# Kernel tuning notes

Hardware: AMD Instinct MI355X
Metric: run time of the kernel (lower is better)

## Reference

```python
import jax, jax.numpy as jnp
import numpy as np

N_MELS = 80
N_MAPS = 128
N_LABELS = 35
INTEGRATION_TIME = 1.0
NSTEPS = 4  # fixed-step RK4 stand-in for adaptive dopri5
BN_EPS = 1e-5


def _conv(x, w, pad_h):
    # x: [B, C, T, 1], w: [O, I, kH, 1]
    return jax.lax.conv_general_dilated(
        x, w, window_strides=(1, 1), padding=[(pad_h, pad_h), (0, 0)],
        dimension_numbers=("NCHW", "OIHW", "NCHW"))


def _bn(x):
    # BatchNorm2d(affine=False) with batch statistics (training-mode math, biased var)
    m = jnp.mean(x, axis=(0, 2, 3), keepdims=True)
    v = jnp.mean(jnp.square(x - m), axis=(0, 2, 3), keepdims=True)
    return (x - m) * jax.lax.rsqrt(v + BN_EPS)


def setup_inputs() -> dict:
    key = jax.random.key(0)
    ks = jax.random.split(key, 7)
    B, T = 128, 500
    def he(k, shape, fan_in):
        return jax.random.normal(k, shape, dtype=jnp.float32) * np.float32(np.sqrt(2.0 / fan_in))
    return {
        "x": jax.random.normal(ks[0], (B, N_MELS, T), dtype=jnp.float32),
        "conv0_w": he(ks[1], (N_MAPS, N_MELS, 3, 1), N_MELS * 3),
        "conv1_w": he(ks[2], (N_MAPS, N_MAPS, 9, 1), N_MAPS * 9),
        "conv2_w": he(ks[3], (N_MAPS, N_MAPS, 9, 1), N_MAPS * 9),
        "conv3_w": he(ks[4], (N_MAPS, N_MAPS, 1, 1), N_MAPS),
        "out_w": he(ks[5], (N_LABELS, N_MAPS), N_MAPS),
        "out_b": jnp.zeros((N_LABELS,), dtype=jnp.float32),
    }


def reference(x, conv0_w, conv1_w, conv2_w, conv3_w, out_w, out_b):
    # x: [B, n_mels, T] -> unsqueeze(3) -> [B, n_mels, T, 1]
    h = x[..., None]
    h = _conv(h, conv0_w, pad_h=1)          # conv0 (3,1), pad (1,0)
    h = jax.nn.relu(_bn(h))                  # norm_in + relu

    def odefunc(z):
        # TCNN_ODEfunc.forward (t only selects BN stats; batch stats used here)
        out = _conv(z, conv1_w, pad_h=4)
        out = jax.nn.relu(_bn(out))
        out = _conv(out, conv2_w, pad_h=4)
        out = _bn(out)
        out3 = jax.nn.relu(_bn(_conv(z, conv3_w, pad_h=0)))
        return jax.nn.relu(out + out3)

    dt = jnp.float32(INTEGRATION_TIME / NSTEPS)

    def rk4_step(z, _):
        k1 = odefunc(z)
        k2 = odefunc(z + 0.5 * dt * k1)
        k3 = odefunc(z + 0.5 * dt * k2)
        k4 = odefunc(z + dt * k3)
        return z + (dt / 6.0) * (k1 + 2.0 * k2 + 2.0 * k3 + k4), None

    h, _ = jax.lax.scan(rk4_step, h, None, length=NSTEPS)

    # global average pool over (T, 1) then linear head
    feat = jnp.mean(h.reshape(h.shape[0], h.shape[1], -1), axis=2)  # [B, n_maps]
    return feat @ out_w.T + out_b
```

## Files before the change

### kernel.cpp

```cpp
#include <hip/hip_runtime.h>
#include <hip/hip_bf16.h>
#include <cstddef>

constexpr int B = 128;
constexpr int T = 500;
constexpr int C = 128;
constexpr int CIN = 80;
constexpr int NL = 35;
constexpr size_t NBCT = (size_t)B * C * T;
constexpr int WPAD = 132;
constexpr int I0 = 96;
constexpr int IPAD0 = 104;
constexpr int NT = 64;
constexpr int NPART = 1024;

typedef __attribute__((ext_vector_type(8))) _Float16 half8;
typedef __attribute__((ext_vector_type(4))) _Float16 half4;
typedef __attribute__((ext_vector_type(4))) float f32x4;

__device__ float g_zA[NBCT];
__device__ float g_zB[NBCT];
__device__ _Float16 g_z16[NBCT];
__device__ _Float16 g_accA[NBCT];
__device__ _Float16 g_accB[NBCT];
__device__ _Float16 g_t1[NBCT];
__device__ _Float16 g_t2[NBCT];
__device__ _Float16 g_t3[NBCT];
__device__ float g_ps1[C * NPART], g_pq1[C * NPART];
__device__ float g_ps2[C * NPART], g_pq2[C * NPART];
__device__ float g_ps3[C * NPART], g_pq3[C * NPART];
__device__ float g_m1[C], g_r1[C], g_m2[C], g_r2[C], g_m3[C], g_r3[C];
__device__ float g_featp[B * 4 * C];
__device__ _Float16 g_w0f[3 * C * I0];
__device__ _Float16 g_w1f[9 * C * C];
__device__ _Float16 g_w2f[9 * C * C];
__device__ _Float16 g_w3f[1 * C * C];

__device__ inline half8 h8zero() {
  half8 v;
#pragma unroll
  for (int j = 0; j < 8; j++) v[j] = (_Float16)0.f;
  return v;
}

__inline__ __device__ float wave_sum(float v) {
  for (int off = 32; off; off >>= 1) v += __shfl_down(v, off);
  return v;
}

__device__ inline void swz_block(int& tile, int& b) {
  int flat = blockIdx.y * 8 + blockIdx.x;
  int swz = (flat & 7) * 128 + (flat >> 3);
  tile = swz & 7;
  b = swz >> 3;
}

template <int KW>
__global__ __launch_bounds__(256) void prep_weights_f16(
    const float* __restrict__ w, _Float16* __restrict__ wf) {
  int idx = blockIdx.x * 256 + threadIdx.x;
  if (idx >= C * C * KW) return;
  int kw = idx % KW;
  int i = (idx / KW) % C;
  int o = idx / (KW * C);
  size_t dst = (((size_t)kw * 16 + (i >> 3)) * C + o) * 8 + (i & 7);
  wf[dst] = (_Float16)w[idx];
}

__global__ __launch_bounds__(256) void prep_w0_f16(
    const float* __restrict__ w, _Float16* __restrict__ wf) {
  int idx = blockIdx.x * 256 + threadIdx.x;
  if (idx >= 3 * C * I0) return;
  int i = idx % I0;
  int o = (idx / I0) % C;
  int kw = idx / (I0 * C);
  float v = 0.f;
  if (i < CIN) v = w[((size_t)o * CIN + i) * 3 + kw];
  wf[((size_t)kw * C + o) * I0 + i] = (_Float16)v;
}

__device__ inline void reduce_one(const float* __restrict__ ps,
                                  const float* __restrict__ pq,
                                  float* __restrict__ om,
                                  float* __restrict__ orr, int c) {
  float s = 0.f, q = 0.f;
  for (int p = threadIdx.x; p < NPART; p += 256) {
    s += ps[c * NPART + p];
    q += pq[c * NPART + p];
  }
  s = wave_sum(s);
  q = wave_sum(q);
  __shared__ float ls[8];
  int wv = threadIdx.x >> 6, ln = threadIdx.x & 63;
  if (ln == 0) { ls[wv] = s; ls[4 + wv] = q; }
  __syncthreads();
  if (threadIdx.x == 0) {
    float S = ls[0] + ls[1] + ls[2] + ls[3];
    float Q = ls[4] + ls[5] + ls[6] + ls[7];
    const float invn = 1.f / 64000.f;
    float m = S * invn;
    float v = Q * invn - m * m;
    om[c] = m;
    orr[c] = rsqrtf(v + 1e-5f);
  }
}

__global__ __launch_bounds__(256) void reduce_stats(
    const float* __restrict__ ps, const float* __restrict__ pq,
    float* __restrict__ om, float* __restrict__ orr) {
  reduce_one(ps, pq, om, orr, blockIdx.x);
}

__global__ __launch_bounds__(256) void reduce_stats2(
    const float* __restrict__ psA, const float* __restrict__ pqA,
    float* __restrict__ omA, float* __restrict__ orA,
    const float* __restrict__ psB, const float* __restrict__ pqB,
    float* __restrict__ omB, float* __restrict__ orB) {
  if (blockIdx.y == 0)
    reduce_one(psA, pqA, omA, orA, blockIdx.x);
  else
    reduce_one(psB, pqB, omB, orB, blockIdx.x);
}

template <int NG, int NTG>
__device__ inline void store_and_stats_f(f32x4 (&dacc)[NG][NTG],
                                         float* __restrict__ outb,
                                         float* __restrict__ ssum,
                                         float* __restrict__ ssq, int tbase,
                                         int og0, int quad, int m15) {
#pragma unroll
  for (int g = 0; g < NG; g++) {
    float rs[4] = {0.f, 0.f, 0.f, 0.f}, rq[4] = {0.f, 0.f, 0.f, 0.f};
#pragma unroll
    for (int tg = 0; tg < NTG; tg++) {
      int t = tbase + tg * 16 + m15;
      bool valid = t < T;
      f32x4 d = dacc[g][tg];
      if (valid)
        *(f32x4*)(outb + (size_t)t * C + (og0 + g) * 16 + quad * 4) = d;
#pragma unroll
      for (int r = 0; r < 4; r++) {
        float v = valid ? d[r] : 0.f;
        rs[r] += v;
        rq[r] += v * v;
      }
    }
#pragma unroll
    for (int sh = 1; sh < 16; sh <<= 1) {
#pragma unroll
      for (int r = 0; r < 4; r++) {
        rs[r] += __shfl_xor(rs[r], sh);
        rq[r] += __shfl_xor(rq[r], sh);
      }
    }
    if (m15 == 0) {
      int o = (og0 + g) * 16 + quad * 4;
#pragma unroll
      for (int r = 0; r < 4; r++) {
        atomicAdd(&ssum[o + r], rs[r]);
        atomicAdd(&ssq[o + r], rq[r]);
      }
    }
  }
}

template <int NG, int NTG>
__device__ inline void store_and_stats_h(f32x4 (&dacc)[NG][NTG],
                                         _Float16* __restrict__ outb,
                                         float* __restrict__ ssum,
                                         float* __restrict__ ssq, int tbase,
                                         int og0, int quad, int m15) {
#pragma unroll
  for (int g = 0; g < NG; g++) {
    float rs[4] = {0.f, 0.f, 0.f, 0.f}, rq[4] = {0.f, 0.f, 0.f, 0.f};
#pragma unroll
    for (int tg = 0; tg < NTG; tg++) {
      int t = tbase + tg * 16 + m15;
      bool valid = t < T;
      f32x4 d = dacc[g][tg];
      if (valid) {
        half4 h;
#pragma unroll
        for (int r = 0; r < 4; r++) h[r] = (_Float16)d[r];
        *(half4*)(outb + (size_t)t * C + (og0 + g) * 16 + quad * 4) = h;
      }
#pragma unroll
      for (int r = 0; r < 4; r++) {
        float v = valid ? d[r] : 0.f;
        rs[r] += v;
        rq[r] += v * v;
      }
    }
#pragma unroll
    for (int sh = 1; sh < 16; sh <<= 1) {
#pragma unroll
      for (int r = 0; r < 4; r++) {
        rs[r] += __shfl_xor(rs[r], sh);
        rq[r] += __shfl_xor(rq[r], sh);
      }
    }
    if (m15 == 0) {
      int o = (og0 + g) * 16 + quad * 4;
#pragma unroll
      for (int r = 0; r < 4; r++) {
        atomicAdd(&ssum[o + r], rs[r]);
        atomicAdd(&ssq[o + r], rq[r]);
      }
    }
  }
}

__global__ __launch_bounds__(256, 4) void conv13f(
    const _Float16* __restrict__ t2g, const _Float16* __restrict__ t3g,
    const float* __restrict__ m2, const float* __restrict__ r2,
    const float* __restrict__ m3, const float* __restrict__ r3,
    const float* __restrict__ zc, _Float16* __restrict__ z16,
    const _Float16* __restrict__ accr, float* __restrict__ zn,
    _Float16* __restrict__ accw, const _Float16* __restrict__ w9,
    const _Float16* __restrict__ w1, _Float16* __restrict__ out1,
    _Float16* __restrict__ out3, float* __restrict__ ps1,
    float* __restrict__ pq1, float* __restrict__ ps3,
    float* __restrict__ pq3, float wacc, float anext, int mode, int initf,
    int finf) {
  constexpr int PAD = 4;
  constexpr int ROWS = NT + 8;
  __shared__ __align__(16) _Float16 sh[ROWS * WPAD];
  __shared__ float ssum1[C], ssq1[C], ssum3[C], ssq3[C];
  __shared__ float sm2[C], sr2[C], sm3[C], sr3[C];

  const int tid = threadIdx.x;
  int tile, b;
  swz_block(tile, b);
  const int t0 = tile * NT;

  if (tid < 128) {
    ssum1[tid] = 0.f; ssq1[tid] = 0.f;
    ssum3[tid] = 0.f; ssq3[tid] = 0.f;
    if (mode) {
      sm2[tid] = m2[tid]; sr2[tid] = r2[tid];
      sm3[tid] = m3[tid]; sr3[tid] = r3[tid];
    }
  }
  __syncthreads();

  for (int e = tid; e < ROWS * 16; e += 256) {
    int r = e >> 4;
    int c8 = e & 15;
    int t = t0 - PAD + r;
    half8 v = h8zero();
    if (t >= 0 && t < T) {
      size_t off = (size_t)b * T * C + (size_t)t * C + c8 * 8;
      if (mode == 0) {
        v = *(const half8*)(z16 + off);
      } else {
        half8 h2 = *(const half8*)(t2g + off);
        half8 h3 = *(const half8*)(t3g + off);
        float zf[8];
        if (finf) {
          float4 z0 = *(const float4*)(zc + off);
          float4 z1 = *(const float4*)(zc + off + 4);
          zf[0] = z0.x; zf[1] = z0.y; zf[2] = z0.z; zf[3] = z0.w;
          zf[4] = z1.x; zf[5] = z1.y; zf[6] = z1.z; zf[7] = z1.w;
        } else {
          half8 hz = *(const half8*)(z16 + off);
#pragma unroll
          for (int j = 0; j < 8; j++) zf[j] = (float)hz[j];
        }
        half8 ha = h8zero();
        if (!initf) ha = *(const half8*)(accr + off);
        int c = c8 * 8;
        float va[8], zo[8];
#pragma unroll
        for (int j = 0; j < 8; j++) {
          float f2 = (float)h2[j];
          float f3 = (float)h3[j];
          float k = fmaxf((f2 - sm2[c + j]) * sr2[c + j] +
                              fmaxf((f3 - sm3[c + j]) * sr3[c + j], 0.f),
                          0.f);
          va[j] = initf ? wacc * k : (float)ha[j] + wacc * k;
          zo[j] = zf[j] + anext * (finf ? va[j] : k);
          v[j] = (_Float16)zo[j];
        }
        bool owned = (r >= PAD) && (r < PAD + NT);
        if (owned) {
          if (finf) {
            *(float4*)(zn + off) = make_float4(zo[0], zo[1], zo[2], zo[3]);
            *(float4*)(zn + off + 4) = make_float4(zo[4], zo[5], zo[6], zo[7]);
            *(half8*)(z16 + off) = v;
          } else {
            half8 aw;
#pragma unroll
            for (int j = 0; j < 8; j++) aw[j] = (_Float16)va[j];
            *(half8*)(accw + off) = aw;
          }
        }
      }
    }
    *(half8*)&sh[r * WPAD + c8 * 8] = v;
  }
  __syncthreads();

  const int wv = tid >> 6;
  const int lane = tid & 63;
  const int quad = lane >> 4;
  const int m15 = lane & 15;
  const int og0 = wv * 2;

  const half8* __restrict__ A9 = (const half8*)w9;
  const half8* __restrict__ A1 = (const half8*)w1;

  {
    f32x4 d3[2][4];
#pragma unroll
    for (int g = 0; g < 2; g++)
#pragma unroll
      for (int tg = 0; tg < 4; tg++) d3[g][tg] = f32x4{0.f, 0.f, 0.f, 0.f};
#pragma unroll
    for (int ic = 0; ic < 4; ic++) {
      const int kof = ic * 32 + quad * 8;
      half8 af[2];
#pragma unroll
      for (int g = 0; g < 2; g++)
        af[g] = A1[(ic * 4 + quad) * C + (og0 + g) * 16 + m15];
      half8 bf[4];
#pragma unroll
      for (int tg = 0; tg < 4; tg++)
        bf[tg] = *(const half8*)(sh + (tg * 16 + m15 + PAD) * WPAD + kof);
#pragma unroll
      for (int g = 0; g < 2; g++)
#pragma unroll
        for (int tg = 0; tg < 4; tg++)
          d3[g][tg] = __builtin_amdgcn_mfma_f32_16x16x32_f16(
              af[g], bf[tg], d3[g][tg], 0, 0, 0);
    }
    _Float16* __restrict__ o3b = out3 + (size_t)b * T * C;
    store_and_stats_h<2, 4>(d3, o3b, ssum3, ssq3, t0, og0, quad, m15);
  }

  f32x4 d1[2][4];
#pragma unroll
  for (int g = 0; g < 2; g++)
#pragma unroll
    for (int tg = 0; tg < 4; tg++) d1[g][tg] = f32x4{0.f, 0.f, 0.f, 0.f};

  for (int kw = 0; kw < 9; kw++) {
#pragma unroll
    for (int ic = 0; ic < 4; ic++) {
      const int kof = ic * 32 + quad * 8;
      half8 af[2];
#pragma unroll
      for (int g = 0; g < 2; g++)
        af[g] = A9[(kw * 16 + ic * 4 + quad) * C + (og0 + g) * 16 + m15];
      half8 bf[4];
#pragma unroll
      for (int tg = 0; tg < 4; tg++)
        bf[tg] = *(const half8*)(sh + (tg * 16 + m15 + kw) * WPAD + kof);
#pragma unroll
      for (int g = 0; g < 2; g++)
#pragma unroll
        for (int tg = 0; tg < 4; tg++)
          d1[g][tg] = __builtin_amdgcn_mfma_f32_16x16x32_f16(
              af[g], bf[tg], d1[g][tg], 0, 0, 0);
    }
  }

  _Float16* __restrict__ o1b = out1 + (size_t)b * T * C;
  store_and_stats_h<2, 4>(d1, o1b, ssum1, ssq1, t0, og0, quad, m15);
  __syncthreads();
  int p = b * 8 + tile;
  if (tid < 128) {
    ps1[tid * NPART + p] = ssum1[tid];
    pq1[tid * NPART + p] = ssq1[tid];
    ps3[tid * NPART + p] = ssum3[tid];
    pq3[tid * NPART + p] = ssq3[tid];
  }
}

__global__ __launch_bounds__(256, 4) void conv2_bn(
    const _Float16* __restrict__ in, const _Float16* __restrict__ wf,
    const float* __restrict__ bnm, const float* __restrict__ bnr,
    _Float16* __restrict__ out, float* __restrict__ ps,
    float* __restrict__ pq) {
  constexpr int KW = 9, PAD = 4;
  constexpr int ROWS = NT + KW - 1;
  __shared__ __align__(16) _Float16 sh[ROWS * WPAD];
  __shared__ float ssum[C], ssq[C];
  __shared__ float sbm[C], sbr[C];

  const int tid = threadIdx.x;
  int tile, b;
  swz_block(tile, b);
  const int t0 = tile * NT;

  if (tid < 128) {
    sbm[tid] = bnm[tid];
    sbr[tid] = bnr[tid];
    ssum[tid] = 0.f;
    ssq[tid] = 0.f;
  }
  __syncthreads();

  const _Float16* __restrict__ inb = in + (size_t)b * T * C;
  for (int e = tid; e < ROWS * 16; e += 256) {
    int r = e >> 4;
    int c8 = e & 15;
    int t = t0 - PAD + r;
    half8 v = h8zero();
    if (t >= 0 && t < T) {
      half8 u = *(const half8*)(inb + (size_t)t * C + c8 * 8);
      int c = c8 * 8;
#pragma unroll
      for (int j = 0; j < 8; j++) {
        float f = (float)u[j];
        f = fmaxf((f - sbm[c + j]) * sbr[c + j], 0.f);
        v[j] = (_Float16)f;
      }
    }
    *(half8*)&sh[r * WPAD + c8 * 8] = v;
  }
  __syncthreads();

  const int wv = tid >> 6;
  const int lane = tid & 63;
  const int quad = lane >> 4;
  const int m15 = lane & 15;
  const int og0 = wv * 2;

  const half8* __restrict__ Af = (const half8*)wf;

  f32x4 dacc[2][4];
#pragma unroll
  for (int g = 0; g < 2; g++)
#pragma unroll
    for (int tg = 0; tg < 4; tg++) dacc[g][tg] = f32x4{0.f, 0.f, 0.f, 0.f};

  for (int kw = 0; kw < 9; kw++) {
#pragma unroll
    for (int ic = 0; ic < 4; ic++) {
      const int kof = ic * 32 + quad * 8;
      half8 af[2];
#pragma unroll
      for (int g = 0; g < 2; g++)
        af[g] = Af[(kw * 16 + ic * 4 + quad) * C + (og0 + g) * 16 + m15];
      half8 bf[4];
#pragma unroll
      for (int tg = 0; tg < 4; tg++)
        bf[tg] = *(const half8*)(sh + (tg * 16 + m15 + kw) * WPAD + kof);
#pragma unroll
      for (int g = 0; g < 2; g++)
#pragma unroll
        for (int tg = 0; tg < 4; tg++)
          dacc[g][tg] = __builtin_amdgcn_mfma_f32_16x16x32_f16(
              af[g], bf[tg], dacc[g][tg], 0, 0, 0);
    }
  }

  _Float16* __restrict__ outb = out + (size_t)b * T * C;
  store_and_stats_h<2, 4>(dacc, outb, ssum, ssq, t0, og0, quad, m15);
  __syncthreads();
  int p = b * 8 + tile;
  if (tid < 128) {
    ps[tid * NPART + p] = ssum[tid];
    pq[tid * NPART + p] = ssq[tid];
  }
}

__global__ __launch_bounds__(256) void conv0_mfma(
    const float* __restrict__ in, const _Float16* __restrict__ wf,
    float* __restrict__ out, float* __restrict__ ps, float* __restrict__ pq) {
  constexpr int KW = 3, PAD = 1;
  constexpr int ROWS = NT + KW - 1;
  __shared__ __align__(16) _Float16 sh[ROWS * IPAD0];
  __shared__ float ssum[C], ssq[C];

  const int tid = threadIdx.x;
  const int tile = blockIdx.x;
  const int b = blockIdx.y;
  const int t0 = tile * NT;

  if (tid < 128) { ssum[tid] = 0.f; ssq[tid] = 0.f; }
  __syncthreads();

  const float* __restrict__ inb = in + (size_t)b * CIN * T;
  for (int e = tid; e < I0 * ROWS; e += 256) {
    int i = e / ROWS;
    int r = e % ROWS;
    int t = t0 - PAD + r;
    float v = 0.f;
    if (i < CIN && t >= 0 && t < T) v = inb[(size_t)i * T + t];
    sh[r * IPAD0 + i] = (_Float16)v;
  }
  __syncthreads();

  const int wv = tid >> 6;
  const int lane = tid & 63;
  const int quad = lane >> 4;
  const int m15 = lane & 15;
  const int og0 = wv * 2;

  f32x4 dacc[2][4];
#pragma unroll
  for (int g = 0; g < 2; g++)
#pragma unroll
    for (int tg = 0; tg < 4; tg++) dacc[g][tg] = f32x4{0.f, 0.f, 0.f, 0.f};

  for (int kw = 0; kw < KW; kw++) {
    const _Float16* __restrict__ wk = wf + (size_t)kw * C * I0;
#pragma unroll
    for (int ic = 0; ic < 3; ic++) {
      const int kof = ic * 32 + quad * 8;
      half8 af[2];
#pragma unroll
      for (int g = 0; g < 2; g++) {
        size_t off = (size_t)((og0 + g) * 16 + m15) * I0 + kof;
        af[g] = *(const half8*)(wk + off);
      }
      half8 bf[4];
#pragma unroll
      for (int tg = 0; tg < 4; tg++) {
        int off = (tg * 16 + m15 + kw) * IPAD0 + kof;
        bf[tg] = *(const half8*)(sh + off);
      }
#pragma unroll
      for (int g = 0; g < 2; g++)
#pragma unroll
        for (int tg = 0; tg < 4; tg++)
          dacc[g][tg] = __builtin_amdgcn_mfma_f32_16x16x32_f16(
              af[g], bf[tg], dacc[g][tg], 0, 0, 0);
    }
  }

  float* __restrict__ outb = out + (size_t)b * T * C;
  store_and_stats_f<2, 4>(dacc, outb, ssum, ssq, t0, og0, quad, m15);
  __syncthreads();
  int p = b * 8 + tile;
  if (tid < 128) {
    ps[tid * NPART + p] = ssum[tid];
    pq[tid * NPART + p] = ssq[tid];
  }
}

__global__ __launch_bounds__(256) void apply_bn_relu(
    float* __restrict__ x, const float* __restrict__ m,
    const float* __restrict__ r, _Float16* __restrict__ zh) {
  __shared__ float sm[C], sr[C];
  if (threadIdx.x < 128) {
    sm[threadIdx.x] = m[threadIdx.x];
    sr[threadIdx.x] = r[threadIdx.x];
  }
  __syncthreads();
  const size_t total4 = NBCT / 4;
  size_t stride = (size_t)gridDim.x * 256;
  for (size_t i4 = (size_t)blockIdx.x * 256 + threadIdx.x; i4 < total4;
       i4 += stride) {
    int c = (int)((i4 & 31) * 4);
    float4 v = ((float4*)x)[i4];
    v.x = fmaxf((v.x - sm[c]) * sr[c], 0.f);
    v.y = fmaxf((v.y - sm[c + 1]) * sr[c + 1], 0.f);
    v.z = fmaxf((v.z - sm[c + 2]) * sr[c + 2], 0.f);
    v.w = fmaxf((v.w - sm[c + 3]) * sr[c + 3], 0.f);
    ((float4*)x)[i4] = v;
    half4 h;
    h[0] = (_Float16)v.x;
    h[1] = (_Float16)v.y;
    h[2] = (_Float16)v.z;
    h[3] = (_Float16)v.w;
    *(half4*)(zh + i4 * 4) = h;
  }
}

__global__ __launch_bounds__(256) void combine_fin(
    const _Float16* __restrict__ t2, const _Float16* __restrict__ t3,
    const float* __restrict__ m2, const float* __restrict__ r2,
    const float* __restrict__ m3, const float* __restrict__ r3,
    float* __restrict__ z, const _Float16* __restrict__ acc, float wacc,
    float anext) {
  __shared__ float sm2[C], sr2[C], sm3[C], sr3[C];
  if (threadIdx.x < 128) {
    sm2[threadIdx.x] = m2[threadIdx.x];
    sr2[threadIdx.x] = r2[threadIdx.x];
    sm3[threadIdx.x] = m3[threadIdx.x];
    sr3[threadIdx.x] = r3[threadIdx.x];
  }
  __syncthreads();
  const size_t total4 = NBCT / 4;
  size_t stride = (size_t)gridDim.x * 256;
  for (size_t i4 = (size_t)blockIdx.x * 256 + threadIdx.x; i4 < total4;
       i4 += stride) {
    int c = (int)((i4 & 31) * 4);
    size_t off = i4 * 4;
    half4 h2 = *(const half4*)(t2 + off);
    half4 h3 = *(const half4*)(t3 + off);
    half4 ha = *(const half4*)(acc + off);
    float4 vz = *(const float4*)(z + off);
    float vzf[4] = {vz.x, vz.y, vz.z, vz.w};
    float vo[4];
#pragma unroll
    for (int j = 0; j < 4; j++) {
      float f2 = (float)h2[j];
      float f3 = (float)h3[j];
      float k = fmaxf((f2 - sm2[c + j]) * sr2[c + j] +
                          fmaxf((f3 - sm3[c + j]) * sr3[c + j], 0.f),
                      0.f);
      float va = (float)ha[j] + wacc * k;
      vo[j] = vzf[j] + anext * va;
    }
    *(float4*)(z + off) = make_float4(vo[0], vo[1], vo[2], vo[3]);
  }
}

__global__ __launch_bounds__(256) void feat_part(
    const float* __restrict__ z, float* __restrict__ fp) {
  const int b = blockIdx.x;
  const int s = blockIdx.y;
  const int c = threadIdx.x & 127;
  const int h = threadIdx.x >> 7;
  const float* zb = z + (size_t)b * T * C;
  float sum = 0.f;
  for (int t = s * 125 + h; t < (s + 1) * 125; t += 2)
    sum += zb[(size_t)t * C + c];
  __shared__ float sf[2][C];
  sf[h][c] = sum;
  __syncthreads();
  if (threadIdx.x < 128)
    fp[((size_t)b * 4 + s) * C + threadIdx.x] =
        sf[0][threadIdx.x] + sf[1][threadIdx.x];
}

__global__ __launch_bounds__(256) void head2(
    const float* __restrict__ fp, const float* __restrict__ ow,
    const float* __restrict__ ob, float* __restrict__ out) {
  const int b = blockIdx.x;
  __shared__ float feat[C];
  if (threadIdx.x < 128) {
    float s = 0.f;
#pragma unroll
    for (int p = 0; p < 4; p++) s += fp[((size_t)b * 4 + p) * C + threadIdx.x];
    feat[threadIdx.x] = s * (1.f / 500.f);
  }
  __syncthreads();
  if (threadIdx.x < NL) {
    int l = threadIdx.x;
    float o = ob[l];
    for (int j = 0; j < C; j++) o = fmaf(feat[j], ow[l * C + j], o);
    out[b * NL + l] = o;
  }
}

extern "C" void kernel_launch(void* const* d_in, const int* in_sizes, int n_in,
                              void* d_out, int out_size, void* d_ws,
                              size_t ws_size, hipStream_t stream) {
  const float* x  = (const float*)d_in[0];
  const float* w0 = (const float*)d_in[1];
  const float* w1 = (const float*)d_in[2];
  const float* w2 = (const float*)d_in[3];
  const float* w3 = (const float*)d_in[4];
  const float* ow = (const float*)d_in[5];
  const float* ob = (const float*)d_in[6];
  float* out = (float*)d_out;

  static float *zA, *zB, *featp;
  static float *ps1, *pq1, *ps2, *pq2, *ps3, *pq3;
  static float *m1, *r1, *m2, *r2, *m3, *r3;
  static _Float16 *z16, *accA, *accB, *t1, *t2, *t3;
  static _Float16 *w0f, *w1f, *w2f, *w3f;
  static bool inited = false;
  if (!inited) {
    void* p;
#define GET(sym, var) hipGetSymbolAddress(&p, HIP_SYMBOL(sym)); var = (decltype(var))p;
    GET(g_zA, zA) GET(g_zB, zB) GET(g_z16, z16)
    GET(g_accA, accA) GET(g_accB, accB)
    GET(g_t1, t1) GET(g_t2, t2) GET(g_t3, t3)
    GET(g_ps1, ps1) GET(g_pq1, pq1) GET(g_ps2, ps2) GET(g_pq2, pq2)
    GET(g_ps3, ps3) GET(g_pq3, pq3)
    GET(g_m1, m1) GET(g_r1, r1) GET(g_m2, m2) GET(g_r2, r2)
    GET(g_m3, m3) GET(g_r3, r3) GET(g_featp, featp)
    GET(g_w0f, w0f) GET(g_w1f, w1f) GET(g_w2f, w2f) GET(g_w3f, w3f)
#undef GET
    inited = true;
  }

  prep_w0_f16<<<(3 * C * I0 + 255) / 256, 256, 0, stream>>>(w0, w0f);
  prep_weights_f16<9><<<(C * C * 9 + 255) / 256, 256, 0, stream>>>(w1, w1f);
  prep_weights_f16<9><<<(C * C * 9 + 255) / 256, 256, 0, stream>>>(w2, w2f);
  prep_weights_f16<1><<<(C * C * 1 + 255) / 256, 256, 0, stream>>>(w3, w3f);

  const dim3 convGrid(8, B);
  const int ewGrid = 1024;
  const float dt = 0.25f;

  conv0_mfma<<<dim3(8, B), 256, 0, stream>>>(x, w0f, zA, ps1, pq1);
  reduce_stats<<<C, 256, 0, stream>>>(ps1, pq1, m1, r1);
  apply_bn_relu<<<ewGrid, 256, 0, stream>>>(zA, m1, r1, z16);

  const float waccs[4] = {1.f, 2.f, 2.f, 1.f};
  const float anexts[4] = {0.5f * dt, 0.5f * dt, dt, dt / 6.f};

  float* zcur = zA;
  float* znext = zB;
  _Float16* accbuf[2] = {accA, accB};
  int flip = 0;

  for (int i = 0; i < 16; i++) {
    int sp = (i + 3) % 4;
    int mode = (i == 0) ? 0 : 1;
    int initf = (sp == 0) ? 1 : 0;
    int finf = (sp == 3) ? 1 : 0;
    conv13f<<<convGrid, 256, 0, stream>>>(
        t2, t3, m2, r2, m3, r3, zcur, z16, accbuf[flip], znext,
        accbuf[flip ^ 1], w1f, w3f, t1, t3, ps1, pq1, ps3, pq3,
        mode ? waccs[sp] : 0.f, mode ? anexts[sp] : 0.f, mode, initf, finf);
    if (i >= 1) {
      if (!finf) {
        flip ^= 1;
      } else {
        float* tmp = zcur; zcur = znext; znext = tmp;
      }
    }
    reduce_stats2<<<dim3(C, 2), 256, 0, stream>>>(
        ps1, pq1, m1, r1, ps3, pq3, m3, r3);
    conv2_bn<<<convGrid, 256, 0, stream>>>(
        t1, w2f, m1, r1, t2, ps2, pq2);
    reduce_stats<<<C, 256, 0, stream>>>(ps2, pq2, m2, r2);
  }

  combine_fin<<<ewGrid, 256, 0, stream>>>(
      t2, t3, m2, r2, m3, r3, zcur, accbuf[flip], 1.f, dt / 6.f);

  feat_part<<<dim3(B, 4), 256, 0, stream>>>(zcur, featp);
  head2<<<B, 256, 0, stream>>>(featp, ow, ob, out);
}
```

Measured before the change: 1.424 ms.

## Stage conv outputs through LDS for coalesced stores; fuse final combine into pooling

Conv outputs were previously written straight from MFMA fragments as scattered 8-byte half4 stores. They are now staged in a new shared-memory tile and written back as coalesced 16-byte rows, with the BN statistics computed separately. The last RK combine kernel is folded into the feature pooling kernel, so the final z is never written back to global memory. In exchange the conv kernels use more LDS, which can lower occupancy at launch_bounds(256,4), and they gain extra barriers.

```diff
diff --git a/kernel.cpp b/kernel.cpp
--- a/kernel.cpp
+++ b/kernel.cpp
@@ -123,6 +123,73 @@
 }
 
 template <int NG, int NTG>
+__device__ inline void stats_only(f32x4 (&dacc)[NG][NTG],
+                                  float* __restrict__ ssum,
+                                  float* __restrict__ ssq, int tbase, int og0,
+                                  int quad, int m15) {
+#pragma unroll
+  for (int g = 0; g < NG; g++) {
+    float rs[4] = {0.f, 0.f, 0.f, 0.f}, rq[4] = {0.f, 0.f, 0.f, 0.f};
+#pragma unroll
+    for (int tg = 0; tg < NTG; tg++) {
+      int t = tbase + tg * 16 + m15;
+      bool valid = t < T;
+      f32x4 d = dacc[g][tg];
+#pragma unroll
+      for (int r = 0; r < 4; r++) {
+        float v = valid ? d[r] : 0.f;
+        rs[r] += v;
+        rq[r] += v * v;
+      }
+    }
+#pragma unroll
+    for (int sh = 1; sh < 16; sh <<= 1) {
+#pragma unroll
+      for (int r = 0; r < 4; r++) {
+        rs[r] += __shfl_xor(rs[r], sh);
+        rq[r] += __shfl_xor(rq[r], sh);
+      }
+    }
+    if (m15 == 0) {
+      int o = (og0 + g) * 16 + quad * 4;
+#pragma unroll
+      for (int r = 0; r < 4; r++) {
+        atomicAdd(&ssum[o + r], rs[r]);
+        atomicAdd(&ssq[o + r], rq[r]);
+      }
+    }
+  }
+}
+
+template <int NG, int NTG>
+__device__ inline void frags_to_lds(f32x4 (&dacc)[NG][NTG],
+                                    _Float16* __restrict__ sho, int og0,
+                                    int quad, int m15) {
+#pragma unroll
+  for (int g = 0; g < NG; g++)
+#pragma unroll
+    for (int tg = 0; tg < NTG; tg++) {
+      half4 h;
+#pragma unroll
+      for (int r = 0; r < 4; r++) h[r] = (_Float16)dacc[g][tg][r];
+      *(half4*)&sho[(tg * 16 + m15) * WPAD + (og0 + g) * 16 + quad * 4] = h;
+    }
+}
+
+__device__ inline void lds_to_global_h(const _Float16* __restrict__ sho,
+                                       _Float16* __restrict__ outb, int t0,
+                                       int tid) {
+  for (int e = tid; e < NT * 16; e += 256) {
+    int row = e >> 4;
+    int c8 = e & 15;
+    int t = t0 + row;
+    if (t < T)
+      *(half8*)(outb + (size_t)t * C + c8 * 8) =
+          *(const half8*)&sho[row * WPAD + c8 * 8];
+  }
+}
+
+template <int NG, int NTG>
 __device__ inline void store_and_stats_f(f32x4 (&dacc)[NG][NTG],
                                          float* __restrict__ outb,
                                          float* __restrict__ ssum,
@@ -138,52 +205,6 @@
       f32x4 d = dacc[g][tg];
       if (valid)
         *(f32x4*)(outb + (size_t)t * C + (og0 + g) * 16 + quad * 4) = d;
-#pragma unroll
-      for (int r = 0; r < 4; r++) {
-        float v = valid ? d[r] : 0.f;
-        rs[r] += v;
-        rq[r] += v * v;
-      }
-    }
-#pragma unroll
-    for (int sh = 1; sh < 16; sh <<= 1) {
-#pragma unroll
-      for (int r = 0; r < 4; r++) {
-        rs[r] += __shfl_xor(rs[r], sh);
-        rq[r] += __shfl_xor(rq[r], sh);
-      }
-    }
-    if (m15 == 0) {
-      int o = (og0 + g) * 16 + quad * 4;
-#pragma unroll
-      for (int r = 0; r < 4; r++) {
-        atomicAdd(&ssum[o + r], rs[r]);
-        atomicAdd(&ssq[o + r], rq[r]);
-      }
-    }
-  }
-}
-
-template <int NG, int NTG>
-__device__ inline void store_and_stats_h(f32x4 (&dacc)[NG][NTG],
-                                         _Float16* __restrict__ outb,
-                                         float* __restrict__ ssum,
-                                         float* __restrict__ ssq, int tbase,
-                                         int og0, int quad, int m15) {
-#pragma unroll
-  for (int g = 0; g < NG; g++) {
-    float rs[4] = {0.f, 0.f, 0.f, 0.f}, rq[4] = {0.f, 0.f, 0.f, 0.f};
-#pragma unroll
-    for (int tg = 0; tg < NTG; tg++) {
-      int t = tbase + tg * 16 + m15;
-      bool valid = t < T;
-      f32x4 d = dacc[g][tg];
-      if (valid) {
-        half4 h;
-#pragma unroll
-        for (int r = 0; r < 4; r++) h[r] = (_Float16)d[r];
-        *(half4*)(outb + (size_t)t * C + (og0 + g) * 16 + quad * 4) = h;
-      }
 #pragma unroll
       for (int r = 0; r < 4; r++) {
         float v = valid ? d[r] : 0.f;
@@ -225,6 +246,7 @@
   constexpr int PAD = 4;
   constexpr int ROWS = NT + 8;
   __shared__ __align__(16) _Float16 sh[ROWS * WPAD];
+  __shared__ __align__(16) _Float16 sho[NT * WPAD];
   __shared__ float ssum1[C], ssq1[C], ssum3[C], ssq3[C];
   __shared__ float sm2[C], sr2[C], sm3[C], sr3[C];
 
@@ -308,6 +330,8 @@
 
   const half8* __restrict__ A9 = (const half8*)w9;
   const half8* __restrict__ A1 = (const half8*)w1;
+  _Float16* __restrict__ o1b = out1 + (size_t)b * T * C;
+  _Float16* __restrict__ o3b = out3 + (size_t)b * T * C;
 
   {
     f32x4 d3[2][4];
@@ -333,9 +357,11 @@
           d3[g][tg] = __builtin_amdgcn_mfma_f32_16x16x32_f16(
               af[g], bf[tg], d3[g][tg], 0, 0, 0);
     }
-    _Float16* __restrict__ o3b = out3 + (size_t)b * T * C;
-    store_and_stats_h<2, 4>(d3, o3b, ssum3, ssq3, t0, og0, quad, m15);
-  }
+    frags_to_lds<2, 4>(d3, sho, og0, quad, m15);
+    stats_only<2, 4>(d3, ssum3, ssq3, t0, og0, quad, m15);
+  }
+  __syncthreads();
+  lds_to_global_h(sho, o3b, t0, tid);
 
   f32x4 d1[2][4];
 #pragma unroll
@@ -364,9 +390,12 @@
     }
   }
 
-  _Float16* __restrict__ o1b = out1 + (size_t)b * T * C;
-  store_and_stats_h<2, 4>(d1, o1b, ssum1, ssq1, t0, og0, quad, m15);
-  __syncthreads();
+  __syncthreads();
+  frags_to_lds<2, 4>(d1, sho, og0, quad, m15);
+  stats_only<2, 4>(d1, ssum1, ssq1, t0, og0, quad, m15);
+  __syncthreads();
+  lds_to_global_h(sho, o1b, t0, tid);
+
   int p = b * 8 + tile;
   if (tid < 128) {
     ps1[tid * NPART + p] = ssum1[tid];
@@ -384,6 +413,7 @@
   constexpr int KW = 9, PAD = 4;
   constexpr int ROWS = NT + KW - 1;
   __shared__ __align__(16) _Float16 sh[ROWS * WPAD];
+  __shared__ __align__(16) _Float16 sho[NT * WPAD];
   __shared__ float ssum[C], ssq[C];
   __shared__ float sbm[C], sbr[C];
 
@@ -455,9 +485,12 @@
     }
   }
 
+  frags_to_lds<2, 4>(dacc, sho, og0, quad, m15);
+  stats_only<2, 4>(dacc, ssum, ssq, t0, og0, quad, m15);
+  __syncthreads();
   _Float16* __restrict__ outb = out + (size_t)b * T * C;
-  store_and_stats_h<2, 4>(dacc, outb, ssum, ssq, t0, og0, quad, m15);
-  __syncthreads();
+  lds_to_global_h(sho, outb, t0, tid);
+
   int p = b * 8 + tile;
   if (tid < 128) {
     ps[tid * NPART + p] = ssum[tid];
@@ -569,12 +602,12 @@
   }
 }
 
-__global__ __launch_bounds__(256) void combine_fin(
+__global__ __launch_bounds__(256) void feat_fin(
     const _Float16* __restrict__ t2, const _Float16* __restrict__ t3,
     const float* __restrict__ m2, const float* __restrict__ r2,
     const float* __restrict__ m3, const float* __restrict__ r3,
-    float* __restrict__ z, const _Float16* __restrict__ acc, float wacc,
-    float anext) {
+    const float* __restrict__ z, const _Float16* __restrict__ acc,
+    float wacc, float anext, float* __restrict__ fp) {
   __shared__ float sm2[C], sr2[C], sm3[C], sr3[C];
   if (threadIdx.x < 128) {
     sm2[threadIdx.x] = m2[threadIdx.x];
@@ -583,42 +616,21 @@
     sr3[threadIdx.x] = r3[threadIdx.x];
   }
   __syncthreads();
-  const size_t total4 = NBCT / 4;
-  size_t stride = (size_t)gridDim.x * 256;
-  for (size_t i4 = (size_t)blockIdx.x * 256 + threadIdx.x; i4 < total4;
-       i4 += stride) {
-    int c = (int)((i4 & 31) * 4);
-    size_t off = i4 * 4;
-    half4 h2 = *(const half4*)(t2 + off);
-    half4 h3 = *(const half4*)(t3 + off);
-    half4 ha = *(const half4*)(acc + off);
-    float4 vz = *(const float4*)(z + off);
-    float vzf[4] = {vz.x, vz.y, vz.z, vz.w};
-    float vo[4];
-#pragma unroll
-    for (int j = 0; j < 4; j++) {
-      float f2 = (float)h2[j];
-      float f3 = (float)h3[j];
-      float k = fmaxf((f2 - sm2[c + j]) * sr2[c + j] +
-                          fmaxf((f3 - sm3[c + j]) * sr3[c + j], 0.f),
-                      0.f);
-      float va = (float)ha[j] + wacc * k;
-      vo[j] = vzf[j] + anext * va;
-    }
-    *(float4*)(z + off) = make_float4(vo[0], vo[1], vo[2], vo[3]);
-  }
-}
-
-__global__ __launch_bounds__(256) void feat_part(
-    const float* __restrict__ z, float* __restrict__ fp) {
   const int b = blockIdx.x;
   const int s = blockIdx.y;
   const int c = threadIdx.x & 127;
   const int h = threadIdx.x >> 7;
-  const float* zb = z + (size_t)b * T * C;
   float sum = 0.f;
-  for (int t = s * 125 + h; t < (s + 1) * 125; t += 2)
-    sum += zb[(size_t)t * C + c];
+  for (int t = s * 125 + h; t < (s + 1) * 125; t += 2) {
+    size_t off = (size_t)b * T * C + (size_t)t * C + c;
+    float f2 = (float)t2[off];
+    float f3 = (float)t3[off];
+    float k = fmaxf((f2 - sm2[c]) * sr2[c] +
+                        fmaxf((f3 - sm3[c]) * sr3[c], 0.f),
+                    0.f);
+    float va = (float)acc[off] + wacc * k;
+    sum += z[off] + anext * va;
+  }
   __shared__ float sf[2][C];
   sf[h][c] = sum;
   __syncthreads();
@@ -724,9 +736,7 @@
     reduce_stats<<<C, 256, 0, stream>>>(ps2, pq2, m2, r2);
   }
 
-  combine_fin<<<ewGrid, 256, 0, stream>>>(
-      t2, t3, m2, r2, m3, r3, zcur, accbuf[flip], 1.f, dt / 6.f);
-
-  feat_part<<<dim3(B, 4), 256, 0, stream>>>(zcur, featp);
+  feat_fin<<<dim3(B, 4), 256, 0, stream>>>(
+      t2, t3, m2, r2, m3, r3, zcur, accbuf[flip], 1.f, dt / 6.f, featp);
   head2<<<B, 256, 0, stream>>>(featp, ow, ob, out);
 }
```

After: 1.352 ms. 1.05x faster.

## Transpose BN partial-stat layout and fuse final RK combine into feature pooling

Applied to the files above, without the earlier changes.

The per-block BN partial sums are now stored partition-major ([NPART][C]), so the conv kernels write 128 contiguous floats per block. The reduction reads 16 channels per block with coalesced rows and uses 8 blocks instead of 128. Separately, the final RK4 combine is fused into the average-pool kernel, which avoids writing back the full fp32 state and rereading it. The cost is that each stats reduction now runs on only 8 blocks, which may serialize the 1024-partition sum.

```diff
diff --git a/kernel.cpp b/kernel.cpp
--- a/kernel.cpp
+++ b/kernel.cpp
@@ -26,9 +26,9 @@
 __device__ _Float16 g_t1[NBCT];
 __device__ _Float16 g_t2[NBCT];
 __device__ _Float16 g_t3[NBCT];
-__device__ float g_ps1[C * NPART], g_pq1[C * NPART];
-__device__ float g_ps2[C * NPART], g_pq2[C * NPART];
-__device__ float g_ps3[C * NPART], g_pq3[C * NPART];
+__device__ float g_ps1[NPART * C], g_pq1[NPART * C];
+__device__ float g_ps2[NPART * C], g_pq2[NPART * C];
+__device__ float g_ps3[NPART * C], g_pq3[NPART * C];
 __device__ float g_m1[C], g_r1[C], g_m2[C], g_r2[C], g_m3[C], g_r3[C];
 __device__ float g_featp[B * 4 * C];
 __device__ _Float16 g_w0f[3 * C * I0];
@@ -40,11 +40,6 @@
   half8 v;
 #pragma unroll
   for (int j = 0; j < 8; j++) v[j] = (_Float16)0.f;
-  return v;
-}
-
-__inline__ __device__ float wave_sum(float v) {
-  for (int off = 32; off; off >>= 1) v += __shfl_down(v, off);
   return v;
 }
 
@@ -79,36 +74,41 @@
   wf[((size_t)kw * C + o) * I0 + i] = (_Float16)v;
 }
 
-__device__ inline void reduce_one(const float* __restrict__ ps,
-                                  const float* __restrict__ pq,
-                                  float* __restrict__ om,
-                                  float* __restrict__ orr, int c) {
+__device__ inline void reduce_oneT(const float* __restrict__ ps,
+                                   const float* __restrict__ pq,
+                                   float* __restrict__ om,
+                                   float* __restrict__ orr, int cg) {
+  const int cl = threadIdx.x & 15;
+  const int pr = threadIdx.x >> 4;
+  const int c = cg * 16 + cl;
   float s = 0.f, q = 0.f;
-  for (int p = threadIdx.x; p < NPART; p += 256) {
-    s += ps[c * NPART + p];
-    q += pq[c * NPART + p];
-  }
-  s = wave_sum(s);
-  q = wave_sum(q);
-  __shared__ float ls[8];
-  int wv = threadIdx.x >> 6, ln = threadIdx.x & 63;
-  if (ln == 0) { ls[wv] = s; ls[4 + wv] = q; }
-  __syncthreads();
-  if (threadIdx.x == 0) {
-    float S = ls[0] + ls[1] + ls[2] + ls[3];
-    float Q = ls[4] + ls[5] + ls[6] + ls[7];
+  for (int p = pr; p < NPART; p += 16) {
+    s += ps[(size_t)p * C + c];
+    q += pq[(size_t)p * C + c];
+  }
+  __shared__ float lss[16][17], lsq[16][17];
+  lss[pr][cl] = s;
+  lsq[pr][cl] = q;
+  __syncthreads();
+  if (threadIdx.x < 16) {
+    float S = 0.f, Q = 0.f;
+#pragma unroll
+    for (int r = 0; r < 16; r++) {
+      S += lss[r][threadIdx.x];
+      Q += lsq[r][threadIdx.x];
+    }
     const float invn = 1.f / 64000.f;
     float m = S * invn;
     float v = Q * invn - m * m;
-    om[c] = m;
-    orr[c] = rsqrtf(v + 1e-5f);
+    om[cg * 16 + threadIdx.x] = m;
+    orr[cg * 16 + threadIdx.x] = rsqrtf(v + 1e-5f);
   }
 }
 
 __global__ __launch_bounds__(256) void reduce_stats(
     const float* __restrict__ ps, const float* __restrict__ pq,
     float* __restrict__ om, float* __restrict__ orr) {
-  reduce_one(ps, pq, om, orr, blockIdx.x);
+  reduce_oneT(ps, pq, om, orr, blockIdx.x);
 }
 
 __global__ __launch_bounds__(256) void reduce_stats2(
@@ -117,9 +117,9 @@
     const float* __restrict__ psB, const float* __restrict__ pqB,
     float* __restrict__ omB, float* __restrict__ orB) {
   if (blockIdx.y == 0)
-    reduce_one(psA, pqA, omA, orA, blockIdx.x);
+    reduce_oneT(psA, pqA, omA, orA, blockIdx.x);
   else
-    reduce_one(psB, pqB, omB, orB, blockIdx.x);
+    reduce_oneT(psB, pqB, omB, orB, blockIdx.x);
 }
 
 template <int NG, int NTG>
@@ -369,10 +369,10 @@
   __syncthreads();
   int p = b * 8 + tile;
   if (tid < 128) {
-    ps1[tid * NPART + p] = ssum1[tid];
-    pq1[tid * NPART + p] = ssq1[tid];
-    ps3[tid * NPART + p] = ssum3[tid];
-    pq3[tid * NPART + p] = ssq3[tid];
+    ps1[(size_t)p * C + tid] = ssum1[tid];
+    pq1[(size_t)p * C + tid] = ssq1[tid];
+    ps3[(size_t)p * C + tid] = ssum3[tid];
+    pq3[(size_t)p * C + tid] = ssq3[tid];
   }
 }
 
@@ -460,8 +460,8 @@
   __syncthreads();
   int p = b * 8 + tile;
   if (tid < 128) {
-    ps[tid * NPART + p] = ssum[tid];
-    pq[tid * NPART + p] = ssq[tid];
+    ps[(size_t)p * C + tid] = ssum[tid];
+    pq[(size_t)p * C + tid] = ssq[tid];
   }
 }
 
@@ -535,8 +535,8 @@
   __syncthreads();
   int p = b * 8 + tile;
   if (tid < 128) {
-    ps[tid * NPART + p] = ssum[tid];
-    pq[tid * NPART + p] = ssq[tid];
+    ps[(size_t)p * C + tid] = ssum[tid];
+    pq[(size_t)p * C + tid] = ssq[tid];
   }
 }
 
@@ -569,12 +569,12 @@
   }
 }
 
-__global__ __launch_bounds__(256) void combine_fin(
+__global__ __launch_bounds__(256) void feat_fin(
     const _Float16* __restrict__ t2, const _Float16* __restrict__ t3,
     const float* __restrict__ m2, const float* __restrict__ r2,
     const float* __restrict__ m3, const float* __restrict__ r3,
-    float* __restrict__ z, const _Float16* __restrict__ acc, float wacc,
-    float anext) {
+    const float* __restrict__ z, const _Float16* __restrict__ acc,
+    float wacc, float anext, float* __restrict__ fp) {
   __shared__ float sm2[C], sr2[C], sm3[C], sr3[C];
   if (threadIdx.x < 128) {
     sm2[threadIdx.x] = m2[threadIdx.x];
@@ -583,42 +583,21 @@
     sr3[threadIdx.x] = r3[threadIdx.x];
   }
   __syncthreads();
-  const size_t total4 = NBCT / 4;
-  size_t stride = (size_t)gridDim.x * 256;
-  for (size_t i4 = (size_t)blockIdx.x * 256 + threadIdx.x; i4 < total4;
-       i4 += stride) {
-    int c = (int)((i4 & 31) * 4);
-    size_t off = i4 * 4;
-    half4 h2 = *(const half4*)(t2 + off);
-    half4 h3 = *(const half4*)(t3 + off);
-    half4 ha = *(const half4*)(acc + off);
-    float4 vz = *(const float4*)(z + off);
-    float vzf[4] = {vz.x, vz.y, vz.z, vz.w};
-    float vo[4];
-#pragma unroll
-    for (int j = 0; j < 4; j++) {
-      float f2 = (float)h2[j];
-      float f3 = (float)h3[j];
-      float k = fmaxf((f2 - sm2[c + j]) * sr2[c + j] +
-                          fmaxf((f3 - sm3[c + j]) * sr3[c + j], 0.f),
-                      0.f);
-      float va = (float)ha[j] + wacc * k;
-      vo[j] = vzf[j] + anext * va;
-    }
-    *(float4*)(z + off) = make_float4(vo[0], vo[1], vo[2], vo[3]);
-  }
-}
-
-__global__ __launch_bounds__(256) void feat_part(
-    const float* __restrict__ z, float* __restrict__ fp) {
   const int b = blockIdx.x;
   const int s = blockIdx.y;
   const int c = threadIdx.x & 127;
   const int h = threadIdx.x >> 7;
-  const float* zb = z + (size_t)b * T * C;
   float sum = 0.f;
-  for (int t = s * 125 + h; t < (s + 1) * 125; t += 2)
-    sum += zb[(size_t)t * C + c];
+  for (int t = s * 125 + h; t < (s + 1) * 125; t += 2) {
+    size_t off = (size_t)b * T * C + (size_t)t * C + c;
+    float f2 = (float)t2[off];
+    float f3 = (float)t3[off];
+    float k = fmaxf((f2 - sm2[c]) * sr2[c] +
+                        fmaxf((f3 - sm3[c]) * sr3[c], 0.f),
+                    0.f);
+    float va = (float)acc[off] + wacc * k;
+    sum += z[off] + anext * va;
+  }
   __shared__ float sf[2][C];
   sf[h][c] = sum;
   __syncthreads();
@@ -690,7 +669,7 @@
   const float dt = 0.25f;
 
   conv0_mfma<<<dim3(8, B), 256, 0, stream>>>(x, w0f, zA, ps1, pq1);
-  reduce_stats<<<C, 256, 0, stream>>>(ps1, pq1, m1, r1);
+  reduce_stats<<<dim3(8), 256, 0, stream>>>(ps1, pq1, m1, r1);
   apply_bn_relu<<<ewGrid, 256, 0, stream>>>(zA, m1, r1, z16);
 
   const float waccs[4] = {1.f, 2.f, 2.f, 1.f};
@@ -717,16 +696,14 @@
         float* tmp = zcur; zcur = znext; znext = tmp;
       }
     }
-    reduce_stats2<<<dim3(C, 2), 256, 0, stream>>>(
+    reduce_stats2<<<dim3(8, 2), 256, 0, stream>>>(
         ps1, pq1, m1, r1, ps3, pq3, m3, r3);
     conv2_bn<<<convGrid, 256, 0, stream>>>(
         t1, w2f, m1, r1, t2, ps2, pq2);
-    reduce_stats<<<C, 256, 0, stream>>>(ps2, pq2, m2, r2);
-  }
-
-  combine_fin<<<ewGrid, 256, 0, stream>>>(
-      t2, t3, m2, r2, m3, r3, zcur, accbuf[flip], 1.f, dt / 6.f);
-
-  feat_part<<<dim3(B, 4), 256, 0, stream>>>(zcur, featp);
+    reduce_stats<<<dim3(8), 256, 0, stream>>>(ps2, pq2, m2, r2);
+  }
+
+  feat_fin<<<dim3(B, 4), 256, 0, stream>>>(
+      t2, t3, m2, r2, m3, r3, zcur, accbuf[flip], 1.f, dt / 6.f, featp);
   head2<<<B, 256, 0, stream>>>(featp, ow, ob, out);
 }
```

Measured after the change: 1.857 ms. 30.4% more time.
